# Performance work log

Hardware: AMD Instinct MI355X
Metric: run time of the kernel (lower is better)

## Reference

```python
import jax, jax.numpy as jnp
import numpy as np
import itertools

# Buffers from init_kwargs (constants)
N_GRID = (64, 64, 64)
GRID_MIN = 0.0
DX = 1.0 / 64.0
D, H, W = N_GRID[0] + 2, N_GRID[1] + 2, N_GRID[2] + 2  # padded grid 66^3


def setup_inputs() -> dict:
    key = jax.random.key(0)
    k1, k2, k3, k4 = jax.random.split(key, 4)
    B, N, Ci, Co = 2, 200000, 32, 32
    x = jax.random.normal(k1, (B, N, Ci), jnp.float32)
    # positions uniform in [0,1) -> Xp=(pos-grid_min)/dx in [0,64), indices in [0,65]
    pos = jax.random.uniform(k2, (B, N, 3), jnp.float32)
    kernel = jax.random.normal(k3, (3, 3, 3, Ci, Co), jnp.float32) * 0.1
    bias = jax.random.normal(k4, (Co,), jnp.float32) * 0.1
    return {"x": x, "pos": pos, "kernel": kernel, "bias": bias}


def _forward(x, pos, kernel, bias):
    B, N, Ci = x.shape
    Co = kernel.shape[-1]
    Xp = (pos - GRID_MIN) / DX                      # [B,N,3]
    base = Xp.astype(jnp.int32)                     # trunc == floor (Xp >= 0)
    fx = Xp - base.astype(Xp.dtype) - 0.5
    # quadratic B-spline weights: w[..., k, dim], k in {0,1,2}
    w = jnp.stack([0.5 * (0.5 - fx) ** 2,
                   0.75 - fx ** 2,
                   0.5 * (0.5 + fx) ** 2], axis=-2)  # [B,N,3,3]
    base = base + 1
    batch = jnp.arange(B)[:, None]                  # [B,1] for batched scatter
    result = jnp.zeros((B, D * H * W, Co), x.dtype)
    # 27 fixed stencil offsets (structural small loop, not a data-dim loop)
    for oi, oj, ok in itertools.product(range(3), repeat=3):
        weight = w[..., oi, 0] * w[..., oj, 1] * w[..., ok, 2]      # [B,N]
        idx = base + jnp.array([oi, oj, ok], jnp.int32) - 1          # [B,N,3]
        idx1d = idx[..., 0] * (H * W) + idx[..., 1] * W + idx[..., 2]
        vals = weight[..., None] * (x @ kernel[oi, oj, ok] + bias)   # [B,N,Co]
        result = result.at[batch, idx1d].add(vals)
    return result.reshape(B, D, H, W, Co).transpose(0, 4, 1, 2, 3)   # [B,Co,D,H,W]


def reference(x, pos, kernel, bias):
    return _forward(x, pos, kernel, bias)
```

## Files before the change

### kernel.cpp

```cpp
#include <hip/hip_runtime.h>

#define GD   66
#define GHW  (66*66)
#define GDHW (66*66*66)
#define CI   32
#define CO   32

__device__ __forceinline__ void atomAdd(float* p, float v) {
    unsafeAtomicAdd(p, v);
}

template<bool CELLCO>
__global__ __launch_bounds__(256) void p2g_kernel(
    const float* __restrict__ x, const float* __restrict__ pos,
    const float* __restrict__ kern, const float* __restrict__ bias,
    float* __restrict__ dst, int N, int nPairs)
{
    __shared__ float kl[9*32*32];
    const int co   = threadIdx.x & 31;
    const int half = threadIdx.x >> 5;
    const float bco = bias[co];
    const int halvesTotal = gridDim.x * 8;

    for (int oi = 0; oi < 3; ++oi) {
        __syncthreads();
        for (int i = threadIdx.x; i < 9*32*32; i += 256)
            kl[i] = kern[oi*(9*32*32) + i];
        __syncthreads();

        for (int pp = blockIdx.x*8 + half; pp < nPairs; pp += halvesTotal) {
            const int g0 = pp*2;

            float xr[2][32];
            #pragma unroll
            for (int p = 0; p < 2; ++p) {
                const float4* xp = (const float4*)(x + (size_t)(g0+p)*CI);
                #pragma unroll
                for (int i = 0; i < 8; ++i) {
                    float4 v = xp[i];
                    xr[p][4*i+0]=v.x; xr[p][4*i+1]=v.y; xr[p][4*i+2]=v.z; xr[p][4*i+3]=v.w;
                }
            }

            float wxo[2], wy[2][3], wz[2][3];
            int cb[2], bsel[2];
            #pragma unroll
            for (int p = 0; p < 2; ++p) {
                const int gp = g0 + p;
                float px = pos[gp*3+0]*64.f, py = pos[gp*3+1]*64.f, pz = pos[gp*3+2]*64.f;
                int bx = (int)px, by = (int)py, bz = (int)pz;
                float fx = px - bx - 0.5f, fy = py - by - 0.5f, fz = pz - bz - 0.5f;
                float a0 = 0.5f*(0.5f-fx)*(0.5f-fx);
                float a1 = 0.75f - fx*fx;
                float a2 = 0.5f*(0.5f+fx)*(0.5f+fx);
                wxo[p] = (oi==0) ? a0 : ((oi==1) ? a1 : a2);
                wy[p][0]=0.5f*(0.5f-fy)*(0.5f-fy); wy[p][1]=0.75f-fy*fy; wy[p][2]=0.5f*(0.5f+fy)*(0.5f+fy);
                wz[p][0]=0.5f*(0.5f-fz)*(0.5f-fz); wz[p][1]=0.75f-fz*fz; wz[p][2]=0.5f*(0.5f+fz)*(0.5f+fz);
                cb[p]   = (bx+oi)*GHW + by*GD + bz;
                bsel[p] = (gp >= N) ? 1 : 0;
            }

            #pragma unroll
            for (int oj = 0; oj < 3; ++oj) {
                #pragma unroll
                for (int ok = 0; ok < 3; ++ok) {
                    const float* kc = kl + (oj*3+ok)*1024;
                    float y0 = bco, y1 = bco;
                    #pragma unroll
                    for (int ci = 0; ci < 32; ++ci) {
                        float kv = kc[ci*32 + co];
                        y0 += xr[0][ci]*kv;
                        y1 += xr[1][ci]*kv;
                    }
                    {
                        int cell = cb[0] + oj*GD + ok;
                        float w  = wxo[0]*wy[0][oj]*wz[0][ok];
                        size_t a = CELLCO ? (((size_t)bsel[0]*GDHW + cell)*32 + (size_t)co)
                                          : (((size_t)(bsel[0]*32 + co))*GDHW + (size_t)cell);
                        atomAdd(dst + a, w*y0);
                    }
                    {
                        int cell = cb[1] + oj*GD + ok;
                        float w  = wxo[1]*wy[1][oj]*wz[1][ok];
                        size_t a = CELLCO ? (((size_t)bsel[1]*GDHW + cell)*32 + (size_t)co)
                                          : (((size_t)(bsel[1]*32 + co))*GDHW + (size_t)cell);
                        atomAdd(dst + a, w*y1);
                    }
                }
            }
        }
    }
}

__global__ __launch_bounds__(256) void transp_kernel(
    const float* __restrict__ ws, float* __restrict__ out)
{
    __shared__ float tile[32][33];
    const int b     = blockIdx.y;
    const int cell0 = blockIdx.x * 32;
    const int n     = min(32, GDHW - cell0);

    const float* src = ws + ((size_t)b*GDHW + cell0)*32;
    for (int e = threadIdx.x; e < n*32; e += 256)
        tile[e>>5][e&31] = src[e];
    __syncthreads();
    for (int e = threadIdx.x; e < 32*32; e += 256) {
        int c  = e >> 5;
        int cl = e & 31;
        if (cl < n)
            out[((size_t)(b*32 + c))*GDHW + cell0 + cl] = tile[cl][c];
    }
}

extern "C" void kernel_launch(void* const* d_in, const int* in_sizes, int n_in,
                              void* d_out, int out_size, void* d_ws, size_t ws_size,
                              hipStream_t stream) {
    const float* x    = (const float*)d_in[0];
    const float* pos  = (const float*)d_in[1];
    const float* kern = (const float*)d_in[2];
    const float* bias = (const float*)d_in[3];
    float* out = (float*)d_out;

    const int N  = in_sizes[0] / (2*CI);
    const int BN = 2*N;
    const int nPairs = (BN + 1) / 2;

    const size_t wsNeed = (size_t)2 * GDHW * CO * sizeof(float);

    if (ws_size >= wsNeed) {
        float* ws = (float*)d_ws;
        hipMemsetAsync(ws, 0, wsNeed, stream);
        p2g_kernel<true><<<dim3(2048), dim3(256), 0, stream>>>(x, pos, kern, bias, ws, N, nPairs);
        transp_kernel<<<dim3((GDHW + 31)/32, 2), dim3(256), 0, stream>>>(ws, out);
    } else {
        hipMemsetAsync(out, 0, (size_t)out_size * sizeof(float), stream);
        p2g_kernel<false><<<dim3(2048), dim3(256), 0, stream>>>(x, pos, kern, bias, out, N, nPairs);
    }
}
```

Before: 1.233 ms.

## Hold per-thread kernel slices in registers across nine (oi,oj) passes instead of LDS

Replaces the shared-memory staging of a 9x32x32 kernel slice with per-thread register arrays holding the 3 ok-offsets for one (oi,oj) pair, and restructures the outer loop into 9 passes over the particles. The inner FMA loop then reads weights from registers rather than LDS. In exchange, particle features and positions are reloaded nine times instead of three, and register pressure rises substantially, which may lower occupancy.

Measured after the change: 1.257 ms. About the same (+2.0%).

```diff
diff --git a/kernel.cpp b/kernel.cpp
--- a/kernel.cpp
+++ b/kernel.cpp
@@ -16,17 +16,22 @@
     const float* __restrict__ kern, const float* __restrict__ bias,
     float* __restrict__ dst, int N, int nPairs)
 {
-    __shared__ float kl[9*32*32];
     const int co   = threadIdx.x & 31;
     const int half = threadIdx.x >> 5;
     const float bco = bias[co];
     const int halvesTotal = gridDim.x * 8;
 
-    for (int oi = 0; oi < 3; ++oi) {
-        __syncthreads();
-        for (int i = threadIdx.x; i < 9*32*32; i += 256)
-            kl[i] = kern[oi*(9*32*32) + i];
-        __syncthreads();
+    for (int t = 0; t < 9; ++t) {
+        const int oi = t / 3, oj = t - 3*oi;
+
+        float kreg[3][32];
+        #pragma unroll
+        for (int ok = 0; ok < 3; ++ok) {
+            const float* kp = kern + (size_t)(t*3 + ok)*1024 + co;
+            #pragma unroll
+            for (int ci = 0; ci < 32; ++ci)
+                kreg[ok][ci] = kp[ci*32];
+        }
 
         for (int pp = blockIdx.x*8 + half; pp < nPairs; pp += halvesTotal) {
             const int g0 = pp*2;
@@ -42,7 +47,7 @@
                 }
             }
 
-            float wxo[2], wy[2][3], wz[2][3];
+            float wxy[2], wz[2][3];
             int cb[2], bsel[2];
             #pragma unroll
             for (int p = 0; p < 2; ++p) {
@@ -50,42 +55,45 @@
                 float px = pos[gp*3+0]*64.f, py = pos[gp*3+1]*64.f, pz = pos[gp*3+2]*64.f;
                 int bx = (int)px, by = (int)py, bz = (int)pz;
                 float fx = px - bx - 0.5f, fy = py - by - 0.5f, fz = pz - bz - 0.5f;
-                float a0 = 0.5f*(0.5f-fx)*(0.5f-fx);
-                float a1 = 0.75f - fx*fx;
-                float a2 = 0.5f*(0.5f+fx)*(0.5f+fx);
-                wxo[p] = (oi==0) ? a0 : ((oi==1) ? a1 : a2);
-                wy[p][0]=0.5f*(0.5f-fy)*(0.5f-fy); wy[p][1]=0.75f-fy*fy; wy[p][2]=0.5f*(0.5f+fy)*(0.5f+fy);
+                float wx = (oi==0) ? 0.5f*(0.5f-fx)*(0.5f-fx)
+                         : (oi==1) ? 0.75f - fx*fx
+                                   : 0.5f*(0.5f+fx)*(0.5f+fx);
+                float wy = (oj==0) ? 0.5f*(0.5f-fy)*(0.5f-fy)
+                         : (oj==1) ? 0.75f - fy*fy
+                                   : 0.5f*(0.5f+fy)*(0.5f+fy);
+                wxy[p] = wx*wy;
                 wz[p][0]=0.5f*(0.5f-fz)*(0.5f-fz); wz[p][1]=0.75f-fz*fz; wz[p][2]=0.5f*(0.5f+fz)*(0.5f+fz);
-                cb[p]   = (bx+oi)*GHW + by*GD + bz;
+                cb[p]   = (bx+oi)*GHW + (by+oj)*GD + bz;
                 bsel[p] = (gp >= N) ? 1 : 0;
             }
 
+            float y[3][2];
             #pragma unroll
-            for (int oj = 0; oj < 3; ++oj) {
+            for (int ok = 0; ok < 3; ++ok) { y[ok][0] = bco; y[ok][1] = bco; }
+            #pragma unroll
+            for (int ci = 0; ci < 32; ++ci) {
+                float x0 = xr[0][ci], x1 = xr[1][ci];
                 #pragma unroll
                 for (int ok = 0; ok < 3; ++ok) {
-                    const float* kc = kl + (oj*3+ok)*1024;
-                    float y0 = bco, y1 = bco;
-                    #pragma unroll
-                    for (int ci = 0; ci < 32; ++ci) {
-                        float kv = kc[ci*32 + co];
-                        y0 += xr[0][ci]*kv;
-                        y1 += xr[1][ci]*kv;
-                    }
-                    {
-                        int cell = cb[0] + oj*GD + ok;
-                        float w  = wxo[0]*wy[0][oj]*wz[0][ok];
-                        size_t a = CELLCO ? (((size_t)bsel[0]*GDHW + cell)*32 + (size_t)co)
-                                          : (((size_t)(bsel[0]*32 + co))*GDHW + (size_t)cell);
-                        atomAdd(dst + a, w*y0);
-                    }
-                    {
-                        int cell = cb[1] + oj*GD + ok;
-                        float w  = wxo[1]*wy[1][oj]*wz[1][ok];
-                        size_t a = CELLCO ? (((size_t)bsel[1]*GDHW + cell)*32 + (size_t)co)
-                                          : (((size_t)(bsel[1]*32 + co))*GDHW + (size_t)cell);
-                        atomAdd(dst + a, w*y1);
-                    }
+                    float kv = kreg[ok][ci];
+                    y[ok][0] += x0*kv;
+                    y[ok][1] += x1*kv;
+                }
+            }
+
+            #pragma unroll
+            for (int ok = 0; ok < 3; ++ok) {
+                {
+                    int cell = cb[0] + ok;
+                    size_t a = CELLCO ? (((size_t)bsel[0]*GDHW + cell)*32 + (size_t)co)
+                                      : (((size_t)(bsel[0]*32 + co))*GDHW + (size_t)cell);
+                    atomAdd(dst + a, wxy[0]*wz[0][ok]*y[ok][0]);
+                }
+                {
+                    int cell = cb[1] + ok;
+                    size_t a = CELLCO ? (((size_t)bsel[1]*GDHW + cell)*32 + (size_t)co)
+                                      : (((size_t)(bsel[1]*32 + co))*GDHW + (size_t)cell);
+                    atomAdd(dst + a, wxy[1]*wz[1][ok]*y[ok][1]);
                 }
             }
         }
```
